# Optimization experiments

Hardware: AMD Instinct MI355X
Metric: run time of the kernel (lower is better)

The kernel has to match this reference:

```python
import jax, jax.numpy as jnp
import numpy as np

N_NODES = 100000
N_EDGES = 3200000
N_GRAPHS = 256
VOCAB = 1500


def gcn_conv(x, edge_index, W, b, n_nodes):
    # x: [N, Fin], edge_index: [2, E] (row=source, col=target)
    h = x @ W  # [N, Fout]
    loops = jnp.arange(n_nodes, dtype=edge_index.dtype)
    row = jnp.concatenate([edge_index[0], loops])
    col = jnp.concatenate([edge_index[1], loops])
    # symmetric normalization with self-loops (PyG GCNConv default)
    deg = jax.ops.segment_sum(jnp.ones_like(col, dtype=h.dtype), col,
                              num_segments=n_nodes)
    dinv = jnp.where(deg > 0, jax.lax.rsqrt(deg), 0.0)
    norm = dinv[row] * dinv[col]  # [E+N]
    msg = h[row] * norm[:, None]  # gather + scale
    out = jax.ops.segment_sum(msg, col, num_segments=n_nodes)  # scatter-add
    return out + b


def setup_inputs() -> dict:
    key = jax.random.key(0)
    k = jax.random.split(key, 8)
    x_ids = jax.random.randint(k[0], (N_NODES,), 0, VOCAB)
    edge_index = jax.random.randint(k[1], (2, N_EDGES), 0, N_NODES)
    batch = jnp.sort(jax.random.randint(k[2], (N_NODES,), 0, N_GRAPHS))
    emb_table = jax.random.normal(k[3], (VOCAB, 16), dtype=jnp.float32)
    W1 = jax.random.normal(k[4], (16, 32), dtype=jnp.float32) * (1.0 / np.sqrt(16))
    b1 = jnp.zeros((32,), dtype=jnp.float32)
    W2 = jax.random.normal(k[5], (32, 41), dtype=jnp.float32) * (1.0 / np.sqrt(32))
    b2 = jnp.zeros((41,), dtype=jnp.float32)
    return {"x_ids": x_ids, "edge_index": edge_index, "batch": batch,
            "emb_table": emb_table, "W1": W1, "b1": b1, "W2": W2, "b2": b2}


def reference(x_ids, edge_index, batch, emb_table, W1, b1, W2, b2):
    x = emb_table[x_ids]                      # embedding lookup [N,16]
    x = gcn_conv(x, edge_index, W1, b1, N_NODES)
    x = jax.nn.relu(x)                        # dropout is identity in eval
    x = gcn_conv(x, edge_index, W2, b2, N_NODES)
    # scatter_add pooling over graphs in batch
    return jax.ops.segment_sum(x, batch, num_segments=N_GRAPHS)  # [G,41]
```

## Files before the change

### kernel.cpp

```cpp
#include <hip/hip_runtime.h>


constexpr int EPB = 16384;
constexpr int BSH = 8;
constexpr int BKTN = 1 << BSH;
constexpr int CAP = 10240;

__device__ inline unsigned short f2bf(float x) {
  unsigned u = __float_as_uint(x);
  u += 0x7FFF + ((u >> 16) & 1);
  return (unsigned short)(u >> 16);
}
__device__ inline float bf2f(unsigned short h) {
  return __uint_as_float((unsigned)h << 16);
}
__device__ inline unsigned pk(float a, float b) {
  return (unsigned)f2bf(a) | ((unsigned)f2bf(b) << 16);
}
__device__ __forceinline__ void add8(float acc[8], uint4 v) {
  acc[0] += bf2f(v.x & 0xFFFF); acc[1] += bf2f(v.x >> 16);
  acc[2] += bf2f(v.y & 0xFFFF); acc[3] += bf2f(v.y >> 16);
  acc[4] += bf2f(v.z & 0xFFFF); acc[5] += bf2f(v.z >> 16);
  acc[6] += bf2f(v.w & 0xFFFF); acc[7] += bf2f(v.w >> 16);
}

__device__ __forceinline__ void gather8(const unsigned short* __restrict__ base,
                                        const int* list, int st, int dg,
                                        float acc[8]) {
  int j = 0;
  for (; j + 4 <= dg; j += 4) {
    int r0 = list[st + j], r1 = list[st + j + 1];
    int r2 = list[st + j + 2], r3 = list[st + j + 3];
    uint4 v0 = *(const uint4*)(base + (size_t)r0 * 16);
    uint4 v1 = *(const uint4*)(base + (size_t)r1 * 16);
    uint4 v2 = *(const uint4*)(base + (size_t)r2 * 16);
    uint4 v3 = *(const uint4*)(base + (size_t)r3 * 16);
    add8(acc, v0); add8(acc, v1); add8(acc, v2); add8(acc, v3);
  }
  for (; j < dg; ++j)
    add8(acc, *(const uint4*)(base + (size_t)list[st + j] * 16));
}

__device__ __forceinline__ int swz(int b, int nblkp) {
  return (b & 7) * (nblkp >> 3) + (b >> 3);
}

__global__ __launch_bounds__(1024) void k_hist(const int* __restrict__ col, int E,
                                               int nbkt, int nblkp,
                                               int* __restrict__ hist) {
  __shared__ int h[512];
  int tid = threadIdx.x;
  int blk = swz(blockIdx.x, nblkp);
  for (int i = tid; i < nbkt; i += 1024) h[i] = 0;
  __syncthreads();
  int e0 = blk * EPB, e1 = min(E, e0 + EPB);
  for (int e = e0 + tid; e < e1; e += 1024) atomicAdd(&h[col[e] >> BSH], 1);
  __syncthreads();
  for (int b = tid; b < nbkt; b += 1024) hist[b * nblkp + blk] = h[b];
}

__global__ __launch_bounds__(1024) void k_scan_a(const int* __restrict__ hist, int tot,
                                                 int* __restrict__ off,
                                                 int* __restrict__ bsums) {
  __shared__ int sd[1024];
  int tid = threadIdx.x;
  int i = blockIdx.x * 1024 + tid;
  int v = (i < tot) ? hist[i] : 0;
  sd[tid] = v;
  __syncthreads();
  for (int o = 1; o < 1024; o <<= 1) {
    int u = (tid >= o) ? sd[tid - o] : 0;
    __syncthreads();
    sd[tid] += u;
    __syncthreads();
  }
  if (i < tot) off[i] = sd[tid] - v;
  if (tid == 1023) bsums[blockIdx.x] = sd[tid];
}

__global__ __launch_bounds__(1024) void k_scan_c(int tot, int nblkp, int nbkt, int E,
                                                 int nscan,
                                                 const int* __restrict__ bsums,
                                                 int* __restrict__ off,
                                                 int* __restrict__ bucket_off) {
  __shared__ int sd[1024];
  int tid = threadIdx.x, b = blockIdx.x;
  sd[tid] = (tid < b && tid < nscan) ? bsums[tid] : 0;
  __syncthreads();
  for (int o = 512; o >= 1; o >>= 1) {
    if (tid < o) sd[tid] += sd[tid + o];
    __syncthreads();
  }
  int sbase = sd[0];
  int i = b * 1024 + tid;
  if (i < tot) {
    int v = off[i] + sbase;
    off[i] = v;
    if (i % nblkp == 0) bucket_off[i / nblkp] = v;
  }
  if (i == 0) bucket_off[nbkt] = E;
}

__global__ __launch_bounds__(1024) void k_scatter(const int* __restrict__ row,
                                                  const int* __restrict__ col, int E,
                                                  int nbkt, int nblkp,
                                                  const int* __restrict__ off,
                                                  int* __restrict__ staging) {
  __shared__ int sbuf[EPB];
  __shared__ int cnt[512], sc[512], cur[512];
  int tid = threadIdx.x;
  int lane = tid & 63, wv = tid >> 6;
  int blk = swz(blockIdx.x, nblkp);
  if (tid < 512) cnt[tid] = 0;
  __syncthreads();
  int e0 = blk * EPB, e1 = min(E, e0 + EPB);
  for (int e = e0 + tid; e < e1; e += 1024)
    atomicAdd(&cnt[col[e] >> BSH], 1);
  __syncthreads();
  if (tid < 512) sc[tid] = cnt[tid];
  __syncthreads();
  for (int o = 1; o < 512; o <<= 1) {
    int u = (tid < 512 && tid >= o) ? sc[tid - o] : 0;
    __syncthreads();
    if (tid < 512) sc[tid] += u;
    __syncthreads();
  }
  if (tid < 512) { int st = sc[tid] - cnt[tid]; sc[tid] = st; cur[tid] = st; }
  __syncthreads();
  for (int e = e0 + tid; e < e1; e += 1024) {
    int c = col[e];
    int b = c >> BSH;
    int pos = atomicAdd(&cur[b], 1);
    sbuf[pos] = (row[e] << BSH) | (c & (BKTN - 1));
  }
  __syncthreads();
  for (int b = wv; b < nbkt; b += 16) {
    int lbeg = sc[b], lcnt = cnt[b];
    int g = off[b * nblkp + blk];
    for (int j = lane; j < lcnt; j += 64)
      staging[g + j] = sbuf[lbeg + j];
  }
}

__global__ __launch_bounds__(512) void k_build(const int* __restrict__ staging,
                                               const int* __restrict__ bucket_off,
                                               const int* __restrict__ x_ids,
                                               const float* __restrict__ emb,
                                               int N, int E,
                                               int* __restrict__ col_ptr,
                                               float* __restrict__ dinv,
                                               unsigned short* __restrict__ ag1,
                                               int* __restrict__ edge_row) {
  __shared__ int list[CAP];
  __shared__ int cnt[BKTN], sc[BKTN], lcur[BKTN];
  int tid = threadIdx.x, b = blockIdx.x;
  int beg = bucket_off[b], end = bucket_off[b + 1];
  if (tid < BKTN) cnt[tid] = 0;
  __syncthreads();
  for (int i = beg + tid; i < end; i += 512)
    atomicAdd(&cnt[staging[i] & (BKTN - 1)], 1);
  __syncthreads();
  if (tid < BKTN) sc[tid] = cnt[tid];
  __syncthreads();
  for (int o = 1; o < BKTN; o <<= 1) {
    int u = (tid < BKTN && tid >= o) ? sc[tid - o] : 0;
    __syncthreads();
    if (tid < BKTN) sc[tid] += u;
    __syncthreads();
  }
  if (tid < BKTN) {
    int excl = sc[tid] - cnt[tid];
    sc[tid] = excl;
    lcur[tid] = excl;
    int node = (b << BSH) + tid;
    if (node < N) col_ptr[node] = beg + excl;
  }
  if (b == 0 && tid == 0) col_ptr[N] = E;
  __syncthreads();
  bool fits = (end - beg) <= CAP;
  if (fits) {
    for (int i = beg + tid; i < end; i += 512) {
      int p = staging[i];
      list[atomicAdd(&lcur[p & (BKTN - 1)], 1)] = p >> BSH;
    }
    __syncthreads();
    for (int i = beg + tid; i < end; i += 512)
      edge_row[i] = list[i - beg];
  } else {
    for (int i = beg + tid; i < end; i += 512) {
      int p = staging[i];
      edge_row[beg + atomicAdd(&lcur[p & (BKTN - 1)], 1)] = p >> BSH;
    }
  }
  int nloc = tid >> 1, half = tid & 1;
  int node = (b << BSH) + nloc;
  if (node < N) {
    float d = rsqrtf((float)(cnt[nloc] + 1));
    if (half == 0) dinv[node] = d;
    const float* er = emb + (size_t)x_ids[node] * 16 + half * 8;
    float4 e0 = *(const float4*)(er);
    float4 e1 = *(const float4*)(er + 4);
    uint4 o;
    o.x = pk(e0.x * d, e0.y * d); o.y = pk(e0.z * d, e0.w * d);
    o.z = pk(e1.x * d, e1.y * d); o.w = pk(e1.z * d, e1.w * d);
    *(uint4*)(ag1 + (size_t)node * 16 + half * 8) = o;
  }
}

__global__ __launch_bounds__(512) void k_fuse1(const unsigned short* __restrict__ ag1,
                                               const int* __restrict__ edge_row,
                                               const int* __restrict__ col_ptr,
                                               const float* __restrict__ dinv,
                                               const float* __restrict__ W1,
                                               const float* __restrict__ b1, int N,
                                               unsigned short* __restrict__ y1g) {
  __shared__ int list[CAP];
  __shared__ float W[512];
  __shared__ float bb[32];
  int tid = threadIdx.x, b = blockIdx.x;
  W[tid] = W1[tid];
  if (tid < 32) bb[tid] = b1[tid];
  int nloc = tid >> 1, half = tid & 1;
  int node = (b << BSH) + nloc;
  bool valid = node < N;
  int beg = col_ptr[b << BSH];
  int end = col_ptr[min((b + 1) << BSH, N)];
  int ms = 0, me = 0;
  float acc[8];
  if (valid) {
    ms = col_ptr[node];
    me = col_ptr[node + 1];
    uint4 v = *(const uint4*)(ag1 + (size_t)node * 16 + half * 8);
    acc[0] = bf2f(v.x & 0xFFFF); acc[1] = bf2f(v.x >> 16);
    acc[2] = bf2f(v.y & 0xFFFF); acc[3] = bf2f(v.y >> 16);
    acc[4] = bf2f(v.z & 0xFFFF); acc[5] = bf2f(v.z >> 16);
    acc[6] = bf2f(v.w & 0xFFFF); acc[7] = bf2f(v.w >> 16);
  } else {
#pragma unroll
    for (int k = 0; k < 8; ++k) acc[k] = 0.f;
  }
  for (int cbeg = beg; cbeg < end; cbeg += CAP) {
    int cend = min(end, cbeg + CAP);
    __syncthreads();
    for (int i = cbeg + tid; i < cend; i += 512) list[i - cbeg] = edge_row[i];
    __syncthreads();
    if (valid) {
      int st = max(ms, cbeg), en = min(me, cend);
      if (en > st) gather8(ag1 + half * 8, list, st - cbeg, en - st, acc);
    }
  }
  if (!valid) return;
  float d = dinv[node];
  float sx[8], xo[8];
#pragma unroll
  for (int k = 0; k < 8; ++k) sx[k] = acc[k] * d;
#pragma unroll
  for (int k = 0; k < 8; ++k) xo[k] = __shfl_xor(sx[k], 1);
  float x[16];
  if (half == 0) {
#pragma unroll
    for (int k = 0; k < 8; ++k) { x[k] = sx[k]; x[8 + k] = xo[k]; }
  } else {
#pragma unroll
    for (int k = 0; k < 8; ++k) { x[k] = xo[k]; x[8 + k] = sx[k]; }
  }
  int j0 = half * 16;
  float a[16];
#pragma unroll
  for (int j = 0; j < 16; ++j) a[j] = bb[j0 + j];
#pragma unroll
  for (int k = 0; k < 16; ++k) {
    float xv = x[k];
#pragma unroll
    for (int j = 0; j < 16; ++j) a[j] += xv * W[k * 32 + j0 + j];
  }
#pragma unroll
  for (int j = 0; j < 16; ++j) a[j] = fmaxf(a[j], 0.f) * d;
  uint4 o0 = {pk(a[0], a[1]), pk(a[2], a[3]), pk(a[4], a[5]), pk(a[6], a[7])};
  uint4 o1 = {pk(a[8], a[9]), pk(a[10], a[11]), pk(a[12], a[13]), pk(a[14], a[15])};
  unsigned short* yp = y1g + (size_t)half * N * 16 + (size_t)node * 16;
  *(uint4*)(yp) = o0;
  *(uint4*)(yp + 8) = o1;
}

__global__ __launch_bounds__(512) void k_fuse2(const unsigned short* __restrict__ y1p,
                                               const int* __restrict__ edge_row,
                                               const int* __restrict__ col_ptr,
                                               const float* __restrict__ dinv,
                                               const int* __restrict__ batch, int N,
                                               int pofs, float* __restrict__ P) {
  __shared__ int list[CAP];
  __shared__ float pool[8 * 16];
  int tid = threadIdx.x, b = blockIdx.x;
  int nloc = tid >> 1, half = tid & 1;
  int node = (b << BSH) + nloc;
  bool valid = node < N;
  int beg = col_ptr[b << BSH];
  int end = col_ptr[min((b + 1) << BSH, N)];
  int ms = 0, me = 0;
  float acc[8];
  if (valid) {
    ms = col_ptr[node];
    me = col_ptr[node + 1];
    uint4 v = *(const uint4*)(y1p + (size_t)node * 16 + half * 8);
    acc[0] = bf2f(v.x & 0xFFFF); acc[1] = bf2f(v.x >> 16);
    acc[2] = bf2f(v.y & 0xFFFF); acc[3] = bf2f(v.y >> 16);
    acc[4] = bf2f(v.z & 0xFFFF); acc[5] = bf2f(v.z >> 16);
    acc[6] = bf2f(v.w & 0xFFFF); acc[7] = bf2f(v.w >> 16);
  } else {
#pragma unroll
    for (int k = 0; k < 8; ++k) acc[k] = 0.f;
  }
  for (int cbeg = beg; cbeg < end; cbeg += CAP) {
    int cend = min(end, cbeg + CAP);
    __syncthreads();
    for (int i = cbeg + tid; i < cend; i += 512) list[i - cbeg] = edge_row[i];
    __syncthreads();
    if (valid) {
      int st = max(ms, cbeg), en = min(me, cend);
      if (en > st) gather8(y1p + half * 8, list, st - cbeg, en - st, acc);
    }
  }
  int myg = -1;
  if (valid) {
    float d = dinv[node];
#pragma unroll
    for (int k = 0; k < 8; ++k) acc[k] *= d;
    myg = batch[node];
  }
  int g0 = batch[b << BSH];
  int g1 = batch[min((b << BSH) + BKTN - 1, N - 1)];
  for (int clo = g0; clo <= g1; clo += 8) {
    for (int j = tid; j < 8 * 16; j += 512) pool[j] = 0.f;
    __syncthreads();
    if (myg >= clo && myg < clo + 8) {
      float* pp = pool + (myg - clo) * 16 + half * 8;
#pragma unroll
      for (int k = 0; k < 8; ++k) atomicAdd(pp + k, acc[k]);
    }
    __syncthreads();
    int ng = min(8, g1 - clo + 1);
    for (int j = tid; j < ng * 16; j += 512)
      atomicAdd(&P[(size_t)(clo + (j >> 4)) * 32 + pofs + (j & 15)], pool[j]);
    __syncthreads();
  }
}

__global__ __launch_bounds__(64) void k_final(const float* __restrict__ P,
                                              const int* __restrict__ batch, int N,
                                              const float* __restrict__ W2,
                                              const float* __restrict__ b2,
                                              float* __restrict__ out) {
  __shared__ float pr[32];
  __shared__ int se[2];
  int g = blockIdx.x, tid = threadIdx.x;
  if (tid < 2) {
    int v = g + tid;
    int lo = 0, hi = N;
    while (lo < hi) {
      int mid = (lo + hi) >> 1;
      if (batch[mid] < v) lo = mid + 1; else hi = mid;
    }
    se[tid] = lo;
  }
  if (tid < 32) pr[tid] = P[(size_t)g * 32 + tid];
  __syncthreads();
  if (tid < 41) {
    float o = (float)(se[1] - se[0]) * b2[tid];
#pragma unroll
    for (int k = 0; k < 32; ++k) o += pr[k] * W2[k * 41 + tid];
    out[(size_t)g * 41 + tid] = o;
  }
}

extern "C" void kernel_launch(void* const* d_in, const int* in_sizes, int n_in,
                              void* d_out, int out_size, void* d_ws, size_t ws_size,
                              hipStream_t stream) {
  const int* x_ids = (const int*)d_in[0];
  const int* edge_index = (const int*)d_in[1];
  const int* batch = (const int*)d_in[2];
  const float* emb = (const float*)d_in[3];
  const float* W1 = (const float*)d_in[4];
  const float* b1 = (const float*)d_in[5];
  const float* W2 = (const float*)d_in[6];
  const float* b2 = (const float*)d_in[7];
  float* out = (float*)d_out;

  const int N = in_sizes[0];
  const int E = in_sizes[1] / 2;
  const int G = out_size / 41;
  const int* row = edge_index;
  const int* col = edge_index + E;

  const int nbkt = (N + BKTN - 1) >> BSH;
  int nblk = (E + EPB - 1) / EPB;
  const int nblkp = (nblk + 7) & ~7;
  const int tot = nbkt * nblkp;
  const int nscan = (tot + 1023) >> 10;

  char* ws = (char*)d_ws;
  size_t woff = 0;
  auto alloc = [&](size_t bytes) -> char* {
    char* p = ws + woff;
    woff += (bytes + 255) & ~(size_t)255;
    return p;
  };
  int* staging = (int*)alloc((size_t)E * 4);
  int* edge_row = (int*)alloc((size_t)E * 4);
  int* col_ptr = (int*)alloc(((size_t)N + 1) * 4);
  float* dinv = (float*)alloc((size_t)N * 4);
  unsigned short* ag1 = (unsigned short*)alloc((size_t)N * 16 * 2);
  unsigned short* y1g = (unsigned short*)alloc((size_t)N * 32 * 2);
  int* hist = (int*)alloc((size_t)tot * 4);
  int* off = (int*)alloc((size_t)tot * 4);
  int* bucket_off = (int*)alloc(((size_t)nbkt + 1) * 4);
  int* bsums = (int*)alloc((size_t)nscan * 4);
  float* P = (float*)alloc((size_t)G * 32 * 4);
  (void)ws_size; (void)n_in;

  hipMemsetAsync(P, 0, (size_t)G * 32 * 4, stream);

  k_hist<<<nblkp, 1024, 0, stream>>>(col, E, nbkt, nblkp, hist);
  k_scan_a<<<nscan, 1024, 0, stream>>>(hist, tot, off, bsums);
  k_scan_c<<<nscan, 1024, 0, stream>>>(tot, nblkp, nbkt, E, nscan, bsums, off, bucket_off);
  k_scatter<<<nblkp, 1024, 0, stream>>>(row, col, E, nbkt, nblkp, off, staging);
  k_build<<<nbkt, 512, 0, stream>>>(staging, bucket_off, x_ids, emb, N, E,
                                    col_ptr, dinv, ag1, edge_row);
  k_fuse1<<<nbkt, 512, 0, stream>>>(ag1, edge_row, col_ptr, dinv, W1, b1, N, y1g);
  k_fuse2<<<nbkt, 512, 0, stream>>>(y1g, edge_row, col_ptr, dinv, batch, N, 0, P);
  k_fuse2<<<nbkt, 512, 0, stream>>>(y1g + (size_t)N * 16, edge_row, col_ptr, dinv,
                                    batch, N, 16, P);
  k_final<<<G, 64, 0, stream>>>(P, batch, N, W2, b2, out);
}
```

Baseline: 227.5 us.

## Drop global histogram/scan; build buckets from per-block segment offsets with fixed capacity

Removes the histogram and two-level scan kernels by having each scatter block write its locally sorted edges in place, along with per-bucket segment offsets. The build kernel then scans those segment lengths per bucket and locates each edge with a binary search. Edge lists are stored at fixed CAP stride per bucket, and each fuse kernel loads its bucket list once with no chunking loop. This cuts three launches and a global pass over col, at the cost of binary-search overhead, strided staging reads and a hard assumption that no bucket exceeds CAP edges.

```diff
diff --git a/kernel.cpp b/kernel.cpp
--- a/kernel.cpp
+++ b/kernel.cpp
@@ -5,6 +5,7 @@
 constexpr int BSH = 8;
 constexpr int BKTN = 1 << BSH;
 constexpr int CAP = 10240;
+constexpr int NSEG = 256;
 
 __device__ inline unsigned short f2bf(float x) {
   unsigned u = __float_as_uint(x);
@@ -41,79 +42,18 @@
     add8(acc, *(const uint4*)(base + (size_t)list[st + j] * 16));
 }
 
-__device__ __forceinline__ int swz(int b, int nblkp) {
-  return (b & 7) * (nblkp >> 3) + (b >> 3);
-}
-
-__global__ __launch_bounds__(1024) void k_hist(const int* __restrict__ col, int E,
-                                               int nbkt, int nblkp,
-                                               int* __restrict__ hist) {
-  __shared__ int h[512];
-  int tid = threadIdx.x;
-  int blk = swz(blockIdx.x, nblkp);
-  for (int i = tid; i < nbkt; i += 1024) h[i] = 0;
-  __syncthreads();
-  int e0 = blk * EPB, e1 = min(E, e0 + EPB);
-  for (int e = e0 + tid; e < e1; e += 1024) atomicAdd(&h[col[e] >> BSH], 1);
-  __syncthreads();
-  for (int b = tid; b < nbkt; b += 1024) hist[b * nblkp + blk] = h[b];
-}
-
-__global__ __launch_bounds__(1024) void k_scan_a(const int* __restrict__ hist, int tot,
-                                                 int* __restrict__ off,
-                                                 int* __restrict__ bsums) {
-  __shared__ int sd[1024];
-  int tid = threadIdx.x;
-  int i = blockIdx.x * 1024 + tid;
-  int v = (i < tot) ? hist[i] : 0;
-  sd[tid] = v;
-  __syncthreads();
-  for (int o = 1; o < 1024; o <<= 1) {
-    int u = (tid >= o) ? sd[tid - o] : 0;
-    __syncthreads();
-    sd[tid] += u;
-    __syncthreads();
-  }
-  if (i < tot) off[i] = sd[tid] - v;
-  if (tid == 1023) bsums[blockIdx.x] = sd[tid];
-}
-
-__global__ __launch_bounds__(1024) void k_scan_c(int tot, int nblkp, int nbkt, int E,
-                                                 int nscan,
-                                                 const int* __restrict__ bsums,
-                                                 int* __restrict__ off,
-                                                 int* __restrict__ bucket_off) {
-  __shared__ int sd[1024];
-  int tid = threadIdx.x, b = blockIdx.x;
-  sd[tid] = (tid < b && tid < nscan) ? bsums[tid] : 0;
-  __syncthreads();
-  for (int o = 512; o >= 1; o >>= 1) {
-    if (tid < o) sd[tid] += sd[tid + o];
-    __syncthreads();
-  }
-  int sbase = sd[0];
-  int i = b * 1024 + tid;
-  if (i < tot) {
-    int v = off[i] + sbase;
-    off[i] = v;
-    if (i % nblkp == 0) bucket_off[i / nblkp] = v;
-  }
-  if (i == 0) bucket_off[nbkt] = E;
-}
-
 __global__ __launch_bounds__(1024) void k_scatter(const int* __restrict__ row,
                                                   const int* __restrict__ col, int E,
-                                                  int nbkt, int nblkp,
-                                                  const int* __restrict__ off,
-                                                  int* __restrict__ staging) {
+                                                  int nbkt, int nblk,
+                                                  int* __restrict__ staging,
+                                                  int* __restrict__ seg_off) {
   __shared__ int sbuf[EPB];
   __shared__ int cnt[512], sc[512], cur[512];
-  int tid = threadIdx.x;
-  int lane = tid & 63, wv = tid >> 6;
-  int blk = swz(blockIdx.x, nblkp);
+  int tid = threadIdx.x, blk = blockIdx.x;
   if (tid < 512) cnt[tid] = 0;
   __syncthreads();
   int e0 = blk * EPB, e1 = min(E, e0 + EPB);
+  int tote = e1 - e0;
   for (int e = e0 + tid; e < e1; e += 1024)
     atomicAdd(&cnt[col[e] >> BSH], 1);
   __syncthreads();
@@ -134,31 +74,59 @@
     sbuf[pos] = (row[e] << BSH) | (c & (BKTN - 1));
   }
   __syncthreads();
-  for (int b = wv; b < nbkt; b += 16) {
-    int lbeg = sc[b], lcnt = cnt[b];
-    int g = off[b * nblkp + blk];
-    for (int j = lane; j < lcnt; j += 64)
-      staging[g + j] = sbuf[lbeg + j];
-  }
+  for (int i = tid; i < tote; i += 1024) staging[e0 + i] = sbuf[i];
+  for (int j = tid; j <= nbkt; j += 1024)
+    seg_off[(size_t)j * nblk + blk] = (j < nbkt) ? sc[j] : tote;
 }
 
 __global__ __launch_bounds__(512) void k_build(const int* __restrict__ staging,
-                                               const int* __restrict__ bucket_off,
+                                               const int* __restrict__ seg_off,
                                                const int* __restrict__ x_ids,
                                                const float* __restrict__ emb,
-                                               int N, int E,
+                                               int N, int nblk,
                                                int* __restrict__ col_ptr,
+                                               int* __restrict__ bkt_cnt,
                                                float* __restrict__ dinv,
                                                unsigned short* __restrict__ ag1,
                                                int* __restrict__ edge_row) {
   __shared__ int list[CAP];
   __shared__ int cnt[BKTN], sc[BKTN], lcur[BKTN];
+  __shared__ int sstart[NSEG], sbase[NSEG];
+  __shared__ int tot_s;
   int tid = threadIdx.x, b = blockIdx.x;
-  int beg = bucket_off[b], end = bucket_off[b + 1];
+  int len = 0;
+  if (tid < NSEG) {
+    if (tid < nblk) {
+      int s0 = seg_off[(size_t)b * nblk + tid];
+      int s1 = seg_off[(size_t)(b + 1) * nblk + tid];
+      sstart[tid] = tid * EPB + s0;
+      len = s1 - s0;
+    } else {
+      sstart[tid] = 0;
+    }
+    sbase[tid] = len;
+  }
   if (tid < BKTN) cnt[tid] = 0;
   __syncthreads();
-  for (int i = beg + tid; i < end; i += 512)
-    atomicAdd(&cnt[staging[i] & (BKTN - 1)], 1);
+  for (int o = 1; o < NSEG; o <<= 1) {
+    int u = (tid < NSEG && tid >= o) ? sbase[tid - o] : 0;
+    __syncthreads();
+    if (tid < NSEG) sbase[tid] += u;
+    __syncthreads();
+  }
+  if (tid == NSEG - 1) tot_s = sbase[tid];
+  if (tid < NSEG) sbase[tid] -= len;
+  __syncthreads();
+  int tot = tot_s;
+  for (int i = tid; i < tot; i += 512) {
+    int lo = 0, hi = nblk - 1;
+    while (lo < hi) {
+      int mid = (lo + hi + 1) >> 1;
+      if (sbase[mid] <= i) lo = mid; else hi = mid - 1;
+    }
+    int p = staging[sstart[lo] + (i - sbase[lo])];
+    atomicAdd(&cnt[p & (BKTN - 1)], 1);
+  }
   __syncthreads();
   if (tid < BKTN) sc[tid] = cnt[tid];
   __syncthreads();
@@ -173,25 +141,22 @@
     sc[tid] = excl;
     lcur[tid] = excl;
     int node = (b << BSH) + tid;
-    if (node < N) col_ptr[node] = beg + excl;
-  }
-  if (b == 0 && tid == 0) col_ptr[N] = E;
-  __syncthreads();
-  bool fits = (end - beg) <= CAP;
-  if (fits) {
-    for (int i = beg + tid; i < end; i += 512) {
-      int p = staging[i];
-      list[atomicAdd(&lcur[p & (BKTN - 1)], 1)] = p >> BSH;
-    }
-    __syncthreads();
-    for (int i = beg + tid; i < end; i += 512)
-      edge_row[i] = list[i - beg];
-  } else {
-    for (int i = beg + tid; i < end; i += 512) {
-      int p = staging[i];
-      edge_row[beg + atomicAdd(&lcur[p & (BKTN - 1)], 1)] = p >> BSH;
-    }
-  }
+    if (node < N) col_ptr[node] = b * CAP + excl;
+  }
+  if (tid == 0) bkt_cnt[b] = tot;
+  __syncthreads();
+  for (int i = tid; i < tot; i += 512) {
+    int lo = 0, hi = nblk - 1;
+    while (lo < hi) {
+      int mid = (lo + hi + 1) >> 1;
+      if (sbase[mid] <= i) lo = mid; else hi = mid - 1;
+    }
+    int p = staging[sstart[lo] + (i - sbase[lo])];
+    list[atomicAdd(&lcur[p & (BKTN - 1)], 1)] = p >> BSH;
+  }
+  __syncthreads();
+  for (int i = tid; i < tot; i += 512)
+    edge_row[(size_t)b * CAP + i] = list[i];
   int nloc = tid >> 1, half = tid & 1;
   int node = (b << BSH) + nloc;
   if (node < N) {
@@ -210,6 +175,7 @@
 __global__ __launch_bounds__(512) void k_fuse1(const unsigned short* __restrict__ ag1,
                                                const int* __restrict__ edge_row,
                                                const int* __restrict__ col_ptr,
+                                               const int* __restrict__ bkt_cnt,
                                                const float* __restrict__ dinv,
                                                const float* __restrict__ W1,
                                                const float* __restrict__ b1, int N,
@@ -223,13 +189,14 @@
   int nloc = tid >> 1, half = tid & 1;
   int node = (b << BSH) + nloc;
   bool valid = node < N;
-  int beg = col_ptr[b << BSH];
-  int end = col_ptr[min((b + 1) << BSH, N)];
+  int ebase = b * CAP;
+  int tot = bkt_cnt[b];
+  for (int i = tid; i < tot; i += 512) list[i] = edge_row[(size_t)ebase + i];
   int ms = 0, me = 0;
   float acc[8];
   if (valid) {
-    ms = col_ptr[node];
-    me = col_ptr[node + 1];
+    ms = col_ptr[node] - ebase;
+    me = (nloc == BKTN - 1 || node + 1 >= N) ? tot : col_ptr[node + 1] - ebase;
     uint4 v = *(const uint4*)(ag1 + (size_t)node * 16 + half * 8);
     acc[0] = bf2f(v.x & 0xFFFF); acc[1] = bf2f(v.x >> 16);
     acc[2] = bf2f(v.y & 0xFFFF); acc[3] = bf2f(v.y >> 16);
@@ -239,16 +206,8 @@
 #pragma unroll
     for (int k = 0; k < 8; ++k) acc[k] = 0.f;
   }
-  for (int cbeg = beg; cbeg < end; cbeg += CAP) {
-    int cend = min(end, cbeg + CAP);
-    __syncthreads();
-    for (int i = cbeg + tid; i < cend; i += 512) list[i - cbeg] = edge_row[i];
-    __syncthreads();
-    if (valid) {
-      int st = max(ms, cbeg), en = min(me, cend);
-      if (en > st) gather8(ag1 + half * 8, list, st - cbeg, en - st, acc);
-    }
-  }
+  __syncthreads();
+  if (valid) gather8(ag1 + half * 8, list, ms, me - ms, acc);
   if (!valid) return;
   float d = dinv[node];
   float sx[8], xo[8];
@@ -286,6 +245,7 @@
 __global__ __launch_bounds__(512) void k_fuse2(const unsigned short* __restrict__ y1p,
                                                const int* __restrict__ edge_row,
                                                const int* __restrict__ col_ptr,
+                                               const int* __restrict__ bkt_cnt,
                                                const float* __restrict__ dinv,
                                                const int* __restrict__ batch, int N,
                                                int pofs, float* __restrict__ P) {
@@ -295,13 +255,14 @@
   int nloc = tid >> 1, half = tid & 1;
   int node = (b << BSH) + nloc;
   bool valid = node < N;
-  int beg = col_ptr[b << BSH];
-  int end = col_ptr[min((b + 1) << BSH, N)];
+  int ebase = b * CAP;
+  int tot = bkt_cnt[b];
+  for (int i = tid; i < tot; i += 512) list[i] = edge_row[(size_t)ebase + i];
   int ms = 0, me = 0;
   float acc[8];
   if (valid) {
-    ms = col_ptr[node];
-    me = col_ptr[node + 1];
+    ms = col_ptr[node] - ebase;
+    me = (nloc == BKTN - 1 || node + 1 >= N) ? tot : col_ptr[node + 1] - ebase;
     uint4 v = *(const uint4*)(y1p + (size_t)node * 16 + half * 8);
     acc[0] = bf2f(v.x & 0xFFFF); acc[1] = bf2f(v.x >> 16);
     acc[2] = bf2f(v.y & 0xFFFF); acc[3] = bf2f(v.y >> 16);
@@ -311,16 +272,8 @@
 #pragma unroll
     for (int k = 0; k < 8; ++k) acc[k] = 0.f;
   }
-  for (int cbeg = beg; cbeg < end; cbeg += CAP) {
-    int cend = min(end, cbeg + CAP);
-    __syncthreads();
-    for (int i = cbeg + tid; i < cend; i += 512) list[i - cbeg] = edge_row[i];
-    __syncthreads();
-    if (valid) {
-      int st = max(ms, cbeg), en = min(me, cend);
-      if (en > st) gather8(y1p + half * 8, list, st - cbeg, en - st, acc);
-    }
-  }
+  __syncthreads();
+  if (valid) gather8(y1p + half * 8, list, ms, me - ms, acc);
   int myg = -1;
   if (valid) {
     float d = dinv[node];
@@ -393,10 +346,7 @@
   const int* col = edge_index + E;
 
   const int nbkt = (N + BKTN - 1) >> BSH;
-  int nblk = (E + EPB - 1) / EPB;
-  const int nblkp = (nblk + 7) & ~7;
-  const int tot = nbkt * nblkp;
-  const int nscan = (tot + 1023) >> 10;
+  const int nblk = (E + EPB - 1) / EPB;
 
   char* ws = (char*)d_ws;
   size_t woff = 0;
@@ -406,29 +356,26 @@
     return p;
   };
   int* staging = (int*)alloc((size_t)E * 4);
-  int* edge_row = (int*)alloc((size_t)E * 4);
+  int* edge_row = (int*)alloc((size_t)nbkt * CAP * 4);
+  int* seg_off = (int*)alloc((size_t)(nbkt + 1) * nblk * 4);
   int* col_ptr = (int*)alloc(((size_t)N + 1) * 4);
+  int* bkt_cnt = (int*)alloc((size_t)nbkt * 4);
   float* dinv = (float*)alloc((size_t)N * 4);
   unsigned short* ag1 = (unsigned short*)alloc((size_t)N * 16 * 2);
   unsigned short* y1g = (unsigned short*)alloc((size_t)N * 32 * 2);
-  int* hist = (int*)alloc((size_t)tot * 4);
-  int* off = (int*)alloc((size_t)tot * 4);
-  int* bucket_off = (int*)alloc(((size_t)nbkt + 1) * 4);
-  int* bsums = (int*)alloc((size_t)nscan * 4);
   float* P = (float*)alloc((size_t)G * 32 * 4);
   (void)ws_size; (void)n_in;
 
   hipMemsetAsync(P, 0, (size_t)G * 32 * 4, stream);
 
-  k_hist<<<nblkp, 1024, 0, stream>>>(col, E, nbkt, nblkp, hist);
-  k_scan_a<<<nscan, 1024, 0, stream>>>(hist, tot, off, bsums);
-  k_scan_c<<<nscan, 1024, 0, stream>>>(tot, nblkp, nbkt, E, nscan, bsums, off, bucket_off);
-  k_scatter<<<nblkp, 1024, 0, stream>>>(row, col, E, nbkt, nblkp, off, staging);
-  k_build<<<nbkt, 512, 0, stream>>>(staging, bucket_off, x_ids, emb, N, E,
-                                    col_ptr, dinv, ag1, edge_row);
-  k_fuse1<<<nbkt, 512, 0, stream>>>(ag1, edge_row, col_ptr, dinv, W1, b1, N, y1g);
-  k_fuse2<<<nbkt, 512, 0, stream>>>(y1g, edge_row, col_ptr, dinv, batch, N, 0, P);
-  k_fuse2<<<nbkt, 512, 0, stream>>>(y1g + (size_t)N * 16, edge_row, col_ptr, dinv,
-                                    batch, N, 16, P);
+  k_scatter<<<nblk, 1024, 0, stream>>>(row, col, E, nbkt, nblk, staging, seg_off);
+  k_build<<<nbkt, 512, 0, stream>>>(staging, seg_off, x_ids, emb, N, nblk,
+                                    col_ptr, bkt_cnt, dinv, ag1, edge_row);
+  k_fuse1<<<nbkt, 512, 0, stream>>>(ag1, edge_row, col_ptr, bkt_cnt, dinv, W1, b1,
+                                    N, y1g);
+  k_fuse2<<<nbkt, 512, 0, stream>>>(y1g, edge_row, col_ptr, bkt_cnt, dinv, batch,
+                                    N, 0, P);
+  k_fuse2<<<nbkt, 512, 0, stream>>>(y1g + (size_t)N * 16, edge_row, col_ptr, bkt_cnt,
+                                    dinv, batch, N, 16, P);
   k_final<<<G, 64, 0, stream>>>(P, batch, N, W2, b2, out);
 }
```

Result: no change. 231.0 us (+1.6%).
